# Optimization experiments

Measured on AMD Instinct MI355X. Metric: run time of the kernel, lower is better.

## Reference

```python
import jax, jax.numpy as jnp
from jax import lax
import numpy as np

B, C_IN, C_OUT, K, PAD, H, W = 16, 8, 8, 3, 1, 512, 512
EPS = 1e-5


def setup_inputs() -> dict:
    key = jax.random.key(0)
    k1, k2, k3 = jax.random.split(key, 3)
    x = jax.random.normal(k1, (B, C_IN, H, W), dtype=jnp.float32)
    lin_w = jax.random.normal(k2, (C_IN, C_OUT, K * K), dtype=jnp.float32) * 0.05
    lin_b = jax.random.normal(k3, (C_IN, C_OUT), dtype=jnp.float32) * 0.05
    gamma = jnp.ones((C_OUT,), dtype=jnp.float32)
    beta = jnp.zeros((C_OUT,), dtype=jnp.float32)
    return {"x": x, "lin_w": lin_w, "lin_b": lin_b, "gamma": gamma, "beta": beta}


def reference(x, lin_w, lin_b, gamma, beta):
    # The loop-based im2col + per-channel Linear sum is exactly a conv2d:
    #   kernel[o, c, kh, kw] = lin_w[c, o, kh*K + kw];  bias = sum_c lin_b[c]
    c_in, c_out, kk = lin_w.shape
    k = int(round(kk ** 0.5))
    kernel = jnp.transpose(lin_w, (1, 0, 2)).reshape(c_out, c_in, k, k)  # OIHW
    bias = lin_b.sum(axis=0)  # each Linear adds its own bias; they are summed
    y = lax.conv_general_dilated(
        x, kernel, window_strides=(1, 1), padding=[(PAD, PAD), (PAD, PAD)],
        dimension_numbers=("NCHW", "OIHW", "NCHW"))
    y = y + bias[None, :, None, None]
    # BatchNorm2d (training mode: biased batch statistics over N,H,W) + ReLU
    mean = y.mean(axis=(0, 2, 3), keepdims=True)
    var = y.var(axis=(0, 2, 3), keepdims=True)
    y_hat = (y - mean) * lax.rsqrt(var + EPS)
    out = gamma[None, :, None, None] * y_hat + beta[None, :, None, None]
    return jax.nn.relu(out)
```

## Files before the change

### kernel.cpp

```cpp
#include <hip/hip_runtime.h>
#include <hip/hip_bf16.h>

#define BATCH 16
#define CIN 8
#define COUT 8
#define HH 512
#define WW 512
#define KK 3
constexpr int TPX = 4;
constexpr float EPS = 1e-5f;
constexpr float NPC = (float)BATCH * HH * WW;

template <int MODE>
__global__ __launch_bounds__(256, 4)
void conv_kernel(const float* __restrict__ x,
                 const float* __restrict__ lin_w,
                 const float* __restrict__ gamma,
                 const float* __restrict__ beta,
                 __hip_bfloat16* __restrict__ ws_y,
                 float* __restrict__ stats,
                 float* __restrict__ out) {
    const int w  = blockIdx.x * 256 + threadIdx.x;
    const int h0 = blockIdx.y * TPX;
    const int b  = blockIdx.z;

    float acc[TPX][COUT];
#pragma unroll
    for (int px = 0; px < TPX; ++px)
#pragma unroll
        for (int oc = 0; oc < COUT; ++oc) acc[px][oc] = 0.f;

    const float* xb = x + (size_t)b * CIN * HH * WW;
    const int wm = max(w - 1, 0), wp = min(w + 1, WW - 1);
    const bool wl = (w >= 1), wr = (w <= WW - 2);

    for (int ic = 0; ic < CIN; ++ic) {
        const float* xc = xb + (size_t)ic * HH * WW;
        float xv[TPX + 2][3];
#pragma unroll
        for (int r = 0; r < TPX + 2; ++r) {
            const int hraw = h0 - 1 + r;
            const int hcl = min(max(hraw, 0), HH - 1);
            const bool vr = (hraw >= 0) && (hraw < HH);
            const float* xr = xc + (size_t)hcl * WW;
            float a0 = xr[wm], a1 = xr[w], a2 = xr[wp];
            xv[r][0] = (vr && wl) ? a0 : 0.f;
            xv[r][1] = vr ? a1 : 0.f;
            xv[r][2] = (vr && wr) ? a2 : 0.f;
        }
#pragma unroll
        for (int kh = 0; kh < KK; ++kh) {
#pragma unroll
            for (int kw = 0; kw < KK; ++kw) {
                const int p = kh * KK + kw;
#pragma unroll
                for (int px = 0; px < TPX; ++px) {
                    const float xval = xv[kh + px][kw];
#pragma unroll
                    for (int oc = 0; oc < COUT; ++oc) {
                        acc[px][oc] = fmaf(xval, lin_w[(ic * COUT + oc) * 9 + p],
                                           acc[px][oc]);
                    }
                }
            }
        }
    }

    if (MODE == 0 || MODE == 1) {
        float s[COUT], q[COUT];
#pragma unroll
        for (int oc = 0; oc < COUT; ++oc) {
            float ss = 0.f, qq = 0.f;
#pragma unroll
            for (int px = 0; px < TPX; ++px) {
                ss += acc[px][oc];
                qq = fmaf(acc[px][oc], acc[px][oc], qq);
            }
            s[oc] = ss; q[oc] = qq;
        }
#pragma unroll
        for (int off = 32; off > 0; off >>= 1) {
#pragma unroll
            for (int oc = 0; oc < COUT; ++oc) {
                s[oc] += __shfl_down(s[oc], off);
                q[oc] += __shfl_down(q[oc], off);
            }
        }
        __shared__ float reds[4][2 * COUT];
        const int lane = threadIdx.x & 63, wv = threadIdx.x >> 6;
        if (lane == 0) {
#pragma unroll
            for (int oc = 0; oc < COUT; ++oc) {
                reds[wv][oc] = s[oc];
                reds[wv][COUT + oc] = q[oc];
            }
        }
        __syncthreads();
        if (threadIdx.x < 2 * COUT) {
            float v = reds[0][threadIdx.x] + reds[1][threadIdx.x] +
                      reds[2][threadIdx.x] + reds[3][threadIdx.x];
            atomicAdd(&stats[threadIdx.x], v);
        }
        if (MODE == 0) {
#pragma unroll
            for (int oc = 0; oc < COUT; ++oc)
#pragma unroll
                for (int px = 0; px < TPX; ++px) {
                    size_t oidx = (((size_t)(b * COUT + oc)) * HH + (h0 + px)) * WW + w;
                    ws_y[oidx] = __float2bfloat16(acc[px][oc]);
                }
        }
    } else {
#pragma unroll
        for (int oc = 0; oc < COUT; ++oc) {
            const float mean = stats[oc] * (1.f / NPC);
            const float var  = stats[COUT + oc] * (1.f / NPC) - mean * mean;
            const float rstd = rsqrtf(var + EPS);
            const float sc = gamma[oc] * rstd;
            const float sh = fmaf(-mean, sc, beta[oc]);
#pragma unroll
            for (int px = 0; px < TPX; ++px) {
                size_t oidx = (((size_t)(b * COUT + oc)) * HH + (h0 + px)) * WW + w;
                out[oidx] = fmaxf(fmaf(acc[px][oc], sc, sh), 0.f);
            }
        }
    }
}

__global__ __launch_bounds__(256)
void bn_kernel(const __hip_bfloat16* __restrict__ ws_y,
               const float* __restrict__ stats,
               const float* __restrict__ gamma,
               const float* __restrict__ beta,
               float* __restrict__ out) {
    const size_t i8 = ((size_t)blockIdx.x * 256 + threadIdx.x) * 8;
    const int oc = (int)((i8 >> 18) & 7);
    const float mean = stats[oc] * (1.f / NPC);
    const float var  = stats[COUT + oc] * (1.f / NPC) - mean * mean;
    const float rstd = rsqrtf(var + EPS);
    const float sc = gamma[oc] * rstd;
    const float sh = fmaf(-mean, sc, beta[oc]);

    const uint4 u = *(const uint4*)((const char*)ws_y + i8 * 2);
    float v[8];
    v[0] = __uint_as_float(u.x << 16);
    v[1] = __uint_as_float(u.x & 0xffff0000u);
    v[2] = __uint_as_float(u.y << 16);
    v[3] = __uint_as_float(u.y & 0xffff0000u);
    v[4] = __uint_as_float(u.z << 16);
    v[5] = __uint_as_float(u.z & 0xffff0000u);
    v[6] = __uint_as_float(u.w << 16);
    v[7] = __uint_as_float(u.w & 0xffff0000u);
    float4 o0, o1;
    o0.x = fmaxf(fmaf(v[0], sc, sh), 0.f);
    o0.y = fmaxf(fmaf(v[1], sc, sh), 0.f);
    o0.z = fmaxf(fmaf(v[2], sc, sh), 0.f);
    o0.w = fmaxf(fmaf(v[3], sc, sh), 0.f);
    o1.x = fmaxf(fmaf(v[4], sc, sh), 0.f);
    o1.y = fmaxf(fmaf(v[5], sc, sh), 0.f);
    o1.z = fmaxf(fmaf(v[6], sc, sh), 0.f);
    o1.w = fmaxf(fmaf(v[7], sc, sh), 0.f);
    *(float4*)(out + i8) = o0;
    *(float4*)(out + i8 + 4) = o1;
}

extern "C" void kernel_launch(void* const* d_in, const int* in_sizes, int n_in,
                              void* d_out, int out_size, void* d_ws, size_t ws_size,
                              hipStream_t stream) {
    const float* x     = (const float*)d_in[0];
    const float* lin_w = (const float*)d_in[1];
    const float* gamma = (const float*)d_in[3];
    const float* beta  = (const float*)d_in[4];
    float* out = (float*)d_out;

    float* stats = (float*)d_ws;
    __hip_bfloat16* ws_y = (__hip_bfloat16*)((char*)d_ws + 256);

    const size_t n_elem = (size_t)BATCH * COUT * HH * WW;
    const size_t need = 256 + n_elem * 2;

    hipMemsetAsync(d_ws, 0, 256, stream);

    dim3 grid(WW / 256, HH / TPX, BATCH);
    if (ws_size >= need) {
        conv_kernel<0><<<grid, 256, 0, stream>>>(x, lin_w, gamma, beta, ws_y, stats, out);
        bn_kernel<<<(unsigned)(n_elem / (8 * 256)), 256, 0, stream>>>(ws_y, stats, gamma, beta, out);
    } else {
        conv_kernel<1><<<grid, 256, 0, stream>>>(x, lin_w, gamma, beta, ws_y, stats, out);
        conv_kernel<2><<<grid, 256, 0, stream>>>(x, lin_w, gamma, beta, ws_y, stats, out);
    }
}
```

Measured before the change: 291.9 us.

## Double-buffer input channel loads and use nontemporal stores for outputs

Restructures the conv input loop so the next channel's 3x3 neighbourhood loads are issued before the FMAs on the current channel, using two register buffers. Out-of-range rows are redirected to a zeroed row in the workspace instead of using per-element predicates. Intermediate bf16 and final fp32 stores become nontemporal to avoid polluting cache. The workspace header grows to 4096 bytes to hold the zero row, and the extra buffer raises register pressure.

```diff
diff --git a/kernel.cpp b/kernel.cpp
--- a/kernel.cpp
+++ b/kernel.cpp
@@ -10,6 +10,9 @@
 constexpr int TPX = 4;
 constexpr float EPS = 1e-5f;
 constexpr float NPC = (float)BATCH * HH * WW;
+
+typedef float floatx4 __attribute__((ext_vector_type(4)));
+
 
 template <int MODE>
 __global__ __launch_bounds__(256, 4)
@@ -24,29 +27,45 @@
     const int h0 = blockIdx.y * TPX;
     const int b  = blockIdx.z;
 
-    float acc[TPX][COUT];
-#pragma unroll
-    for (int px = 0; px < TPX; ++px)
-#pragma unroll
-        for (int oc = 0; oc < COUT; ++oc) acc[px][oc] = 0.f;
-
-    const float* xb = x + (size_t)b * CIN * HH * WW;
+    const float* zrow = stats + 65;
+
+    int rowoff[TPX + 2];
+    bool rv[TPX + 2];
+#pragma unroll
+    for (int r = 0; r < TPX + 2; ++r) {
+        const int hraw = h0 - 1 + r;
+        const int hcl = min(max(hraw, 0), HH - 1);
+        rowoff[r] = hcl * WW;
+        rv[r] = (hraw >= 0) && (hraw < HH);
+    }
     const int wm = max(w - 1, 0), wp = min(w + 1, WW - 1);
     const bool wl = (w >= 1), wr = (w <= WW - 2);
-
-    for (int ic = 0; ic < CIN; ++ic) {
-        const float* xc = xb + (size_t)ic * HH * WW;
-        float xv[TPX + 2][3];
+    const float* xb = x + (size_t)b * CIN * HH * WW;
+
+    float acc[TPX][COUT];
+#pragma unroll
+    for (int px = 0; px < TPX; ++px)
+#pragma unroll
+        for (int oc = 0; oc < COUT; ++oc) acc[px][oc] = 0.f;
+
+    float rawA[TPX + 2][3], rawB[TPX + 2][3];
+
+    auto issue = [&](float (&raw)[TPX + 2][3], int ic) {
+        const float* xc = xb + (size_t)ic * (HH * WW);
 #pragma unroll
         for (int r = 0; r < TPX + 2; ++r) {
-            const int hraw = h0 - 1 + r;
-            const int hcl = min(max(hraw, 0), HH - 1);
-            const bool vr = (hraw >= 0) && (hraw < HH);
-            const float* xr = xc + (size_t)hcl * WW;
-            float a0 = xr[wm], a1 = xr[w], a2 = xr[wp];
-            xv[r][0] = (vr && wl) ? a0 : 0.f;
-            xv[r][1] = vr ? a1 : 0.f;
-            xv[r][2] = (vr && wr) ? a2 : 0.f;
+            const float* xr = rv[r] ? (xc + rowoff[r]) : zrow;
+            raw[r][0] = xr[wm];
+            raw[r][1] = xr[w];
+            raw[r][2] = xr[wp];
+        }
+    };
+
+    auto fmab = [&](float (&raw)[TPX + 2][3], int ic) {
+#pragma unroll
+        for (int r = 0; r < TPX + 2; ++r) {
+            raw[r][0] = wl ? raw[r][0] : 0.f;
+            raw[r][2] = wr ? raw[r][2] : 0.f;
         }
 #pragma unroll
         for (int kh = 0; kh < KK; ++kh) {
@@ -55,7 +74,7 @@
                 const int p = kh * KK + kw;
 #pragma unroll
                 for (int px = 0; px < TPX; ++px) {
-                    const float xval = xv[kh + px][kw];
+                    const float xval = raw[kh + px][kw];
 #pragma unroll
                     for (int oc = 0; oc < COUT; ++oc) {
                         acc[px][oc] = fmaf(xval, lin_w[(ic * COUT + oc) * 9 + p],
@@ -64,6 +83,14 @@
                 }
             }
         }
+    };
+
+    issue(rawA, 0);
+    for (int icp = 0; icp < CIN / 2; ++icp) {
+        issue(rawB, 2 * icp + 1);
+        fmab(rawA, 2 * icp);
+        if (icp < CIN / 2 - 1) issue(rawA, 2 * icp + 2);
+        fmab(rawB, 2 * icp + 1);
     }
 
     if (MODE == 0 || MODE == 1) {
@@ -107,7 +134,10 @@
 #pragma unroll
                 for (int px = 0; px < TPX; ++px) {
                     size_t oidx = (((size_t)(b * COUT + oc)) * HH + (h0 + px)) * WW + w;
-                    ws_y[oidx] = __float2bfloat16(acc[px][oc]);
+                    __hip_bfloat16 bv = __float2bfloat16(acc[px][oc]);
+                    __builtin_nontemporal_store(
+                        *(const unsigned short*)&bv,
+                        (unsigned short*)(ws_y + oidx));
                 }
         }
     } else {
@@ -121,7 +151,8 @@
 #pragma unroll
             for (int px = 0; px < TPX; ++px) {
                 size_t oidx = (((size_t)(b * COUT + oc)) * HH + (h0 + px)) * WW + w;
-                out[oidx] = fmaxf(fmaf(acc[px][oc], sc, sh), 0.f);
+                __builtin_nontemporal_store(
+                    fmaxf(fmaf(acc[px][oc], sc, sh), 0.f), out + oidx);
             }
         }
     }
@@ -151,7 +182,7 @@
     v[5] = __uint_as_float(u.z & 0xffff0000u);
     v[6] = __uint_as_float(u.w << 16);
     v[7] = __uint_as_float(u.w & 0xffff0000u);
-    float4 o0, o1;
+    floatx4 o0, o1;
     o0.x = fmaxf(fmaf(v[0], sc, sh), 0.f);
     o0.y = fmaxf(fmaf(v[1], sc, sh), 0.f);
     o0.z = fmaxf(fmaf(v[2], sc, sh), 0.f);
@@ -160,8 +191,8 @@
     o1.y = fmaxf(fmaf(v[5], sc, sh), 0.f);
     o1.z = fmaxf(fmaf(v[6], sc, sh), 0.f);
     o1.w = fmaxf(fmaf(v[7], sc, sh), 0.f);
-    *(float4*)(out + i8) = o0;
-    *(float4*)(out + i8 + 4) = o1;
+    __builtin_nontemporal_store(o0, (floatx4*)(out + i8));
+    __builtin_nontemporal_store(o1, (floatx4*)(out + i8 + 4));
 }
 
 extern "C" void kernel_launch(void* const* d_in, const int* in_sizes, int n_in,
@@ -174,12 +205,12 @@
     float* out = (float*)d_out;
 
     float* stats = (float*)d_ws;
-    __hip_bfloat16* ws_y = (__hip_bfloat16*)((char*)d_ws + 256);
+    __hip_bfloat16* ws_y = (__hip_bfloat16*)((char*)d_ws + 4096);
 
     const size_t n_elem = (size_t)BATCH * COUT * HH * WW;
-    const size_t need = 256 + n_elem * 2;
-
-    hipMemsetAsync(d_ws, 0, 256, stream);
+    const size_t need = 4096 + n_elem * 2;
+
+    hipMemsetAsync(d_ws, 0, 4096, stream);
 
     dim3 grid(WW / 256, HH / TPX, BATCH);
     if (ws_size >= need) {
```

New measurement: 303.4 us. 1.04x slower.

## Tile conv threads horizontally with float4 input loads and packed bf16 stores

Applied to the files above, without the earlier changes.

Reassigns each thread from four vertically stacked pixels to four horizontally adjacent pixels in one row. Input rows are read as one float4 plus two halo scalars, and the intermediate bf16 output is written as packed 8-byte stores (float4 in the fallback path). This cuts load and store instruction counts and widens memory transactions, at the cost of losing vertical reuse of input rows within a thread.

```diff
diff --git a/kernel.cpp b/kernel.cpp
--- a/kernel.cpp
+++ b/kernel.cpp
@@ -6,10 +6,13 @@
 #define COUT 8
 #define HH 512
 #define WW 512
-#define KK 3
-constexpr int TPX = 4;
 constexpr float EPS = 1e-5f;
 constexpr float NPC = (float)BATCH * HH * WW;
+
+static __device__ __forceinline__ unsigned short f2bf(float f) {
+    __hip_bfloat16 h = __float2bfloat16(f);
+    return *reinterpret_cast<unsigned short*>(&h);
+}
 
 template <int MODE>
 __global__ __launch_bounds__(256, 4)
@@ -20,42 +23,50 @@
                  __hip_bfloat16* __restrict__ ws_y,
                  float* __restrict__ stats,
                  float* __restrict__ out) {
-    const int w  = blockIdx.x * 256 + threadIdx.x;
-    const int h0 = blockIdx.y * TPX;
+    const int tw = threadIdx.x & 127;
+    const int w0 = tw * 4;
+    const int h  = blockIdx.y * 2 + (threadIdx.x >> 7);
     const int b  = blockIdx.z;
 
-    float acc[TPX][COUT];
-#pragma unroll
-    for (int px = 0; px < TPX; ++px)
+    float acc[4][COUT];
+#pragma unroll
+    for (int px = 0; px < 4; ++px)
 #pragma unroll
         for (int oc = 0; oc < COUT; ++oc) acc[px][oc] = 0.f;
 
     const float* xb = x + (size_t)b * CIN * HH * WW;
-    const int wm = max(w - 1, 0), wp = min(w + 1, WW - 1);
-    const bool wl = (w >= 1), wr = (w <= WW - 2);
+    const bool wl = (w0 > 0);
+    const bool wr = (w0 + 4 < WW);
+    const int  wm = wl ? w0 - 1 : 0;
+    const int  wp = wr ? w0 + 4 : WW - 1;
 
     for (int ic = 0; ic < CIN; ++ic) {
         const float* xc = xb + (size_t)ic * HH * WW;
-        float xv[TPX + 2][3];
-#pragma unroll
-        for (int r = 0; r < TPX + 2; ++r) {
-            const int hraw = h0 - 1 + r;
+        float xv[3][6];
+#pragma unroll
+        for (int r = 0; r < 3; ++r) {
+            const int hraw = h - 1 + r;
             const int hcl = min(max(hraw, 0), HH - 1);
             const bool vr = (hraw >= 0) && (hraw < HH);
             const float* xr = xc + (size_t)hcl * WW;
-            float a0 = xr[wm], a1 = xr[w], a2 = xr[wp];
-            xv[r][0] = (vr && wl) ? a0 : 0.f;
-            xv[r][1] = vr ? a1 : 0.f;
-            xv[r][2] = (vr && wr) ? a2 : 0.f;
-        }
-#pragma unroll
-        for (int kh = 0; kh < KK; ++kh) {
-#pragma unroll
-            for (int kw = 0; kw < KK; ++kw) {
-                const int p = kh * KK + kw;
-#pragma unroll
-                for (int px = 0; px < TPX; ++px) {
-                    const float xval = xv[kh + px][kw];
+            const float4 v = *(const float4*)(xr + w0);
+            const float  a = xr[wm];
+            const float  c = xr[wp];
+            xv[r][0] = (vr && wl) ? a : 0.f;
+            xv[r][1] = vr ? v.x : 0.f;
+            xv[r][2] = vr ? v.y : 0.f;
+            xv[r][3] = vr ? v.z : 0.f;
+            xv[r][4] = vr ? v.w : 0.f;
+            xv[r][5] = (vr && wr) ? c : 0.f;
+        }
+#pragma unroll
+        for (int kh = 0; kh < 3; ++kh) {
+#pragma unroll
+            for (int kw = 0; kw < 3; ++kw) {
+                const int p = kh * 3 + kw;
+#pragma unroll
+                for (int px = 0; px < 4; ++px) {
+                    const float xval = xv[kh][px + kw];
 #pragma unroll
                     for (int oc = 0; oc < COUT; ++oc) {
                         acc[px][oc] = fmaf(xval, lin_w[(ic * COUT + oc) * 9 + p],
@@ -72,7 +83,7 @@
         for (int oc = 0; oc < COUT; ++oc) {
             float ss = 0.f, qq = 0.f;
 #pragma unroll
-            for (int px = 0; px < TPX; ++px) {
+            for (int px = 0; px < 4; ++px) {
                 ss += acc[px][oc];
                 qq = fmaf(acc[px][oc], acc[px][oc], qq);
             }
@@ -103,12 +114,13 @@
         }
         if (MODE == 0) {
 #pragma unroll
-            for (int oc = 0; oc < COUT; ++oc)
-#pragma unroll
-                for (int px = 0; px < TPX; ++px) {
-                    size_t oidx = (((size_t)(b * COUT + oc)) * HH + (h0 + px)) * WW + w;
-                    ws_y[oidx] = __float2bfloat16(acc[px][oc]);
-                }
+            for (int oc = 0; oc < COUT; ++oc) {
+                size_t oidx = (((size_t)(b * COUT + oc)) * HH + h) * WW + w0;
+                uint2 pk;
+                pk.x = ((unsigned)f2bf(acc[1][oc]) << 16) | f2bf(acc[0][oc]);
+                pk.y = ((unsigned)f2bf(acc[3][oc]) << 16) | f2bf(acc[2][oc]);
+                *(uint2*)(ws_y + oidx) = pk;
+            }
         }
     } else {
 #pragma unroll
@@ -118,11 +130,13 @@
             const float rstd = rsqrtf(var + EPS);
             const float sc = gamma[oc] * rstd;
             const float sh = fmaf(-mean, sc, beta[oc]);
-#pragma unroll
-            for (int px = 0; px < TPX; ++px) {
-                size_t oidx = (((size_t)(b * COUT + oc)) * HH + (h0 + px)) * WW + w;
-                out[oidx] = fmaxf(fmaf(acc[px][oc], sc, sh), 0.f);
-            }
+            size_t oidx = (((size_t)(b * COUT + oc)) * HH + h) * WW + w0;
+            float4 o;
+            o.x = fmaxf(fmaf(acc[0][oc], sc, sh), 0.f);
+            o.y = fmaxf(fmaf(acc[1][oc], sc, sh), 0.f);
+            o.z = fmaxf(fmaf(acc[2][oc], sc, sh), 0.f);
+            o.w = fmaxf(fmaf(acc[3][oc], sc, sh), 0.f);
+            *(float4*)(out + oidx) = o;
         }
     }
 }
@@ -181,7 +195,7 @@
 
     hipMemsetAsync(d_ws, 0, 256, stream);
 
-    dim3 grid(WW / 256, HH / TPX, BATCH);
+    dim3 grid(1, HH / 2, BATCH);
     if (ws_size >= need) {
         conv_kernel<0><<<grid, 256, 0, stream>>>(x, lin_w, gamma, beta, ws_y, stats, out);
         bn_kernel<<<(unsigned)(n_elem / (8 * 256)), 256, 0, stream>>>(ws_y, stats, gamma, beta, out);
```

Measured after the change: 301.8 us. 1.03x slower.

## Fuse conv, stats and BN apply into one cooperative persistent kernel

Applied to the files above, without the earlier changes.

Replaces the conv-plus-stats kernel and the separate BN elementwise kernel with one cooperative kernel of 1024 persistent blocks. Each block loops over 4 virtual tiles and accumulates statistics in registers, so it issues one set of atomics per block instead of one per tile. After a grid-wide sync it applies the normalisation with a grid-stride loop. This removes one kernel launch and the launch gap, at the cost of a grid sync and a smaller grid that may hide latency less well.

```diff
diff --git a/kernel.cpp b/kernel.cpp
--- a/kernel.cpp
+++ b/kernel.cpp
@@ -1,15 +1,156 @@
 #include <hip/hip_runtime.h>
 #include <hip/hip_bf16.h>
+#include <hip/hip_cooperative_groups.h>
+
+namespace cg = cooperative_groups;
 
 #define BATCH 16
 #define CIN 8
 #define COUT 8
 #define HH 512
 #define WW 512
-#define KK 3
 constexpr int TPX = 4;
 constexpr float EPS = 1e-5f;
 constexpr float NPC = (float)BATCH * HH * WW;
+constexpr int NBLK = 1024;
+constexpr int NVIRT = 2 * (HH / TPX) * BATCH;
+constexpr int SUBT = NVIRT / NBLK;
+
+__global__ __launch_bounds__(256, 4)
+void fused_kernel(const float* __restrict__ x,
+                  const float* __restrict__ lin_w,
+                  const float* __restrict__ gamma,
+                  const float* __restrict__ beta,
+                  __hip_bfloat16* __restrict__ ws_y,
+                  float* __restrict__ stats,
+                  float* __restrict__ out) {
+    float s[COUT], q[COUT];
+#pragma unroll
+    for (int oc = 0; oc < COUT; ++oc) { s[oc] = 0.f; q[oc] = 0.f; }
+
+    for (int t = 0; t < SUBT; ++t) {
+        const int v  = blockIdx.x * SUBT + t;
+        const int wx = v & 1;
+        const int hy = (v >> 1) & 127;
+        const int b  = v >> 8;
+        const int w  = wx * 256 + threadIdx.x;
+        const int h0 = hy * TPX;
+
+        float acc[TPX][COUT];
+#pragma unroll
+        for (int px = 0; px < TPX; ++px)
+#pragma unroll
+            for (int oc = 0; oc < COUT; ++oc) acc[px][oc] = 0.f;
+
+        const float* xb = x + (size_t)b * CIN * HH * WW;
+        const int wm = max(w - 1, 0), wp = min(w + 1, WW - 1);
+        const bool wl = (w >= 1), wr = (w <= WW - 2);
+
+        for (int ic = 0; ic < CIN; ++ic) {
+            const float* xc = xb + (size_t)ic * HH * WW;
+            float xv[TPX + 2][3];
+#pragma unroll
+            for (int r = 0; r < TPX + 2; ++r) {
+                const int hraw = h0 - 1 + r;
+                const int hcl = min(max(hraw, 0), HH - 1);
+                const bool vr = (hraw >= 0) && (hraw < HH);
+                const float* xr = xc + (size_t)hcl * WW;
+                float a0 = xr[wm], a1 = xr[w], a2 = xr[wp];
+                xv[r][0] = (vr && wl) ? a0 : 0.f;
+                xv[r][1] = vr ? a1 : 0.f;
+                xv[r][2] = (vr && wr) ? a2 : 0.f;
+            }
+#pragma unroll
+            for (int kh = 0; kh < 3; ++kh) {
+#pragma unroll
+                for (int kw = 0; kw < 3; ++kw) {
+                    const int p = kh * 3 + kw;
+#pragma unroll
+                    for (int px = 0; px < TPX; ++px) {
+                        const float xval = xv[kh + px][kw];
+#pragma unroll
+                        for (int oc = 0; oc < COUT; ++oc) {
+                            acc[px][oc] = fmaf(xval, lin_w[(ic * COUT + oc) * 9 + p],
+                                               acc[px][oc]);
+                        }
+                    }
+                }
+            }
+        }
+
+#pragma unroll
+        for (int oc = 0; oc < COUT; ++oc) {
+#pragma unroll
+            for (int px = 0; px < TPX; ++px) {
+                s[oc] += acc[px][oc];
+                q[oc] = fmaf(acc[px][oc], acc[px][oc], q[oc]);
+                size_t oidx = (((size_t)(b * COUT + oc)) * HH + (h0 + px)) * WW + w;
+                ws_y[oidx] = __float2bfloat16(acc[px][oc]);
+            }
+        }
+    }
+
+#pragma unroll
+    for (int off = 32; off > 0; off >>= 1) {
+#pragma unroll
+        for (int oc = 0; oc < COUT; ++oc) {
+            s[oc] += __shfl_down(s[oc], off);
+            q[oc] += __shfl_down(q[oc], off);
+        }
+    }
+    __shared__ float reds[4][2 * COUT];
+    const int lane = threadIdx.x & 63, wv = threadIdx.x >> 6;
+    if (lane == 0) {
+#pragma unroll
+        for (int oc = 0; oc < COUT; ++oc) {
+            reds[wv][oc] = s[oc];
+            reds[wv][COUT + oc] = q[oc];
+        }
+    }
+    __syncthreads();
+    if (threadIdx.x < 2 * COUT) {
+        float vsum = reds[0][threadIdx.x] + reds[1][threadIdx.x] +
+                     reds[2][threadIdx.x] + reds[3][threadIdx.x];
+        atomicAdd(&stats[threadIdx.x], vsum);
+    }
+
+    cg::this_grid().sync();
+
+    const size_t base = ((size_t)blockIdx.x * 256 + threadIdx.x) * 8;
+    const size_t stride = (size_t)NBLK * 256 * 8;
+    const int oc = (int)((base >> 18) & 7);
+    const volatile float* vst = stats;
+    const float mean = vst[oc] * (1.f / NPC);
+    const float var  = vst[COUT + oc] * (1.f / NPC) - mean * mean;
+    const float rstd = rsqrtf(var + EPS);
+    const float sc = gamma[oc] * rstd;
+    const float sh = fmaf(-mean, sc, beta[oc]);
+
+    const size_t n_elem = (size_t)BATCH * COUT * HH * WW;
+    for (size_t i8 = base; i8 < n_elem; i8 += stride) {
+        const uint4 u = *(const uint4*)((const char*)ws_y + i8 * 2);
+        float v[8];
+        v[0] = __uint_as_float(u.x << 16);
+        v[1] = __uint_as_float(u.x & 0xffff0000u);
+        v[2] = __uint_as_float(u.y << 16);
+        v[3] = __uint_as_float(u.y & 0xffff0000u);
+        v[4] = __uint_as_float(u.z << 16);
+        v[5] = __uint_as_float(u.z & 0xffff0000u);
+        v[6] = __uint_as_float(u.w << 16);
+        v[7] = __uint_as_float(u.w & 0xffff0000u);
+        float4 o0, o1;
+        o0.x = fmaxf(fmaf(v[0], sc, sh), 0.f);
+        o0.y = fmaxf(fmaf(v[1], sc, sh), 0.f);
+        o0.z = fmaxf(fmaf(v[2], sc, sh), 0.f);
+        o0.w = fmaxf(fmaf(v[3], sc, sh), 0.f);
+        o1.x = fmaxf(fmaf(v[4], sc, sh), 0.f);
+        o1.y = fmaxf(fmaf(v[5], sc, sh), 0.f);
+        o1.z = fmaxf(fmaf(v[6], sc, sh), 0.f);
+        o1.w = fmaxf(fmaf(v[7], sc, sh), 0.f);
+        *(float4*)(out + i8) = o0;
+        *(float4*)(out + i8 + 4) = o1;
+    }
+}
 
 template <int MODE>
 __global__ __launch_bounds__(256, 4)
@@ -49,24 +190,22 @@
             xv[r][2] = (vr && wr) ? a2 : 0.f;
         }
 #pragma unroll
-        for (int kh = 0; kh < KK; ++kh) {
-#pragma unroll
-            for (int kw = 0; kw < KK; ++kw) {
-                const int p = kh * KK + kw;
+        for (int kh = 0; kh < 3; ++kh)
+#pragma unroll
+            for (int kw = 0; kw < 3; ++kw) {
+                const int p = kh * 3 + kw;
 #pragma unroll
                 for (int px = 0; px < TPX; ++px) {
                     const float xval = xv[kh + px][kw];
 #pragma unroll
-                    for (int oc = 0; oc < COUT; ++oc) {
+                    for (int oc = 0; oc < COUT; ++oc)
                         acc[px][oc] = fmaf(xval, lin_w[(ic * COUT + oc) * 9 + p],
                                            acc[px][oc]);
-                    }
                 }
             }
-        }
-    }
-
-    if (MODE == 0 || MODE == 1) {
+    }
+
+    if (MODE == 1) {
         float s[COUT], q[COUT];
 #pragma unroll
         for (int oc = 0; oc < COUT; ++oc) {
@@ -79,36 +218,25 @@
             s[oc] = ss; q[oc] = qq;
         }
 #pragma unroll
-        for (int off = 32; off > 0; off >>= 1) {
+        for (int off = 32; off > 0; off >>= 1)
 #pragma unroll
             for (int oc = 0; oc < COUT; ++oc) {
                 s[oc] += __shfl_down(s[oc], off);
                 q[oc] += __shfl_down(q[oc], off);
             }
-        }
         __shared__ float reds[4][2 * COUT];
         const int lane = threadIdx.x & 63, wv = threadIdx.x >> 6;
-        if (lane == 0) {
+        if (lane == 0)
 #pragma unroll
             for (int oc = 0; oc < COUT; ++oc) {
                 reds[wv][oc] = s[oc];
                 reds[wv][COUT + oc] = q[oc];
             }
-        }
         __syncthreads();
         if (threadIdx.x < 2 * COUT) {
-            float v = reds[0][threadIdx.x] + reds[1][threadIdx.x] +
-                      reds[2][threadIdx.x] + reds[3][threadIdx.x];
-            atomicAdd(&stats[threadIdx.x], v);
-        }
-        if (MODE == 0) {
-#pragma unroll
-            for (int oc = 0; oc < COUT; ++oc)
-#pragma unroll
-                for (int px = 0; px < TPX; ++px) {
-                    size_t oidx = (((size_t)(b * COUT + oc)) * HH + (h0 + px)) * WW + w;
-                    ws_y[oidx] = __float2bfloat16(acc[px][oc]);
-                }
+            float vsum = reds[0][threadIdx.x] + reds[1][threadIdx.x] +
+                         reds[2][threadIdx.x] + reds[3][threadIdx.x];
+            atomicAdd(&stats[threadIdx.x], vsum);
         }
     } else {
 #pragma unroll
@@ -125,43 +253,6 @@
             }
         }
     }
-}
-
-__global__ __launch_bounds__(256)
-void bn_kernel(const __hip_bfloat16* __restrict__ ws_y,
-               const float* __restrict__ stats,
-               const float* __restrict__ gamma,
-               const float* __restrict__ beta,
-               float* __restrict__ out) {
-    const size_t i8 = ((size_t)blockIdx.x * 256 + threadIdx.x) * 8;
-    const int oc = (int)((i8 >> 18) & 7);
-    const float mean = stats[oc] * (1.f / NPC);
-    const float var  = stats[COUT + oc] * (1.f / NPC) - mean * mean;
-    const float rstd = rsqrtf(var + EPS);
-    const float sc = gamma[oc] * rstd;
-    const float sh = fmaf(-mean, sc, beta[oc]);
-
-    const uint4 u = *(const uint4*)((const char*)ws_y + i8 * 2);
-    float v[8];
-    v[0] = __uint_as_float(u.x << 16);
-    v[1] = __uint_as_float(u.x & 0xffff0000u);
-    v[2] = __uint_as_float(u.y << 16);
-    v[3] = __uint_as_float(u.y & 0xffff0000u);
-    v[4] = __uint_as_float(u.z << 16);
-    v[5] = __uint_as_float(u.z & 0xffff0000u);
-    v[6] = __uint_as_float(u.w << 16);
-    v[7] = __uint_as_float(u.w & 0xffff0000u);
-    float4 o0, o1;
-    o0.x = fmaxf(fmaf(v[0], sc, sh), 0.f);
-    o0.y = fmaxf(fmaf(v[1], sc, sh), 0.f);
-    o0.z = fmaxf(fmaf(v[2], sc, sh), 0.f);
-    o0.w = fmaxf(fmaf(v[3], sc, sh), 0.f);
-    o1.x = fmaxf(fmaf(v[4], sc, sh), 0.f);
-    o1.y = fmaxf(fmaf(v[5], sc, sh), 0.f);
-    o1.z = fmaxf(fmaf(v[6], sc, sh), 0.f);
-    o1.w = fmaxf(fmaf(v[7], sc, sh), 0.f);
-    *(float4*)(out + i8) = o0;
-    *(float4*)(out + i8 + 4) = o1;
 }
 
 extern "C" void kernel_launch(void* const* d_in, const int* in_sizes, int n_in,
@@ -174,18 +265,24 @@
     float* out = (float*)d_out;
 
     float* stats = (float*)d_ws;
-    __hip_bfloat16* ws_y = (__hip_bfloat16*)((char*)d_ws + 256);
+    __hip_bfloat16* ws_y = (__hip_bfloat16*)((char*)d_ws + 4096);
 
     const size_t n_elem = (size_t)BATCH * COUT * HH * WW;
-    const size_t need = 256 + n_elem * 2;
-
-    hipMemsetAsync(d_ws, 0, 256, stream);
-
-    dim3 grid(WW / 256, HH / TPX, BATCH);
+    const size_t need = 4096 + n_elem * 2;
+
+    (void)hipMemsetAsync(d_ws, 0, 256, stream);
+
+    bool done = false;
     if (ws_size >= need) {
-        conv_kernel<0><<<grid, 256, 0, stream>>>(x, lin_w, gamma, beta, ws_y, stats, out);
-        bn_kernel<<<(unsigned)(n_elem / (8 * 256)), 256, 0, stream>>>(ws_y, stats, gamma, beta, out);
-    } else {
+        void* args[7] = {(void*)&x, (void*)&lin_w, (void*)&gamma, (void*)&beta,
+                         (void*)&ws_y, (void*)&stats, (void*)&out};
+        hipError_t ce = hipLaunchCooperativeKernel(
+            reinterpret_cast<void*>(fused_kernel), dim3(NBLK), dim3(256),
+            args, 0, stream);
+        done = (ce == hipSuccess);
+    }
+    if (!done) {
+        dim3 grid(WW / 256, HH / TPX, BATCH);
         conv_kernel<1><<<grid, 256, 0, stream>>>(x, lin_w, gamma, beta, ws_y, stats, out);
         conv_kernel<2><<<grid, 256, 0, stream>>>(x, lin_w, gamma, beta, ws_y, stats, out);
     }
```

Result: slower. 444.6 us (+52.3%).
